# Optimization experiments

Measured on AMD Instinct MI355X. Metric: run time of the kernel, lower is better.

The kernel has to match this reference:

```python
import jax, jax.numpy as jnp
import numpy as np

N_NODES = 50000
N_EDGES = 800000
F_IN = 64
F_OUT = 64
EPS = 1e-5


def setup_inputs() -> dict:
    key = jax.random.key(0)
    ks = jax.random.split(key, 6)
    x = jax.random.normal(ks[0], (N_NODES, F_IN), dtype=jnp.float32)
    edge_index = jax.random.randint(ks[1], (2, N_EDGES), 0, N_NODES, dtype=jnp.int64)
    # pre MLP: Linear(2*F_in -> F_in); post MLP: Linear(13*F_in -> F_out); lin: Linear(F_out -> F_out)
    pre_w = jax.random.normal(ks[2], (2 * F_IN, F_IN), dtype=jnp.float32) / np.sqrt(2 * F_IN)
    pre_b = jnp.zeros((F_IN,), dtype=jnp.float32)
    post_w = jax.random.normal(ks[3], (13 * F_IN, F_OUT), dtype=jnp.float32) / np.sqrt(13 * F_IN)
    post_b = jnp.zeros((F_OUT,), dtype=jnp.float32)
    lin_w = jax.random.normal(ks[4], (F_OUT, F_OUT), dtype=jnp.float32) / np.sqrt(F_OUT)
    lin_b = jnp.zeros((F_OUT,), dtype=jnp.float32)
    return {"x": x, "edge_index": edge_index, "pre_w": pre_w, "pre_b": pre_b,
            "post_w": post_w, "post_b": post_b, "lin_w": lin_w, "lin_b": lin_b}


def _pna_conv(x, edge_index, pre_w, pre_b, post_w, post_b, lin_w, lin_b):
    n = x.shape[0]
    src = edge_index[0]  # x_j (source / neighbor)
    dst = edge_index[1]  # x_i (target / aggregation index)

    # message: pre-MLP on [x_i, x_j]  -> [E, F_in]
    h = jnp.concatenate([x[dst], x[src]], axis=-1)  # [E, 2*F_in]
    m = h @ pre_w + pre_b                            # [E, F_in]

    # degree of each target node
    deg = jax.ops.segment_sum(jnp.ones_like(src, dtype=x.dtype), dst, num_segments=n)  # [N]
    has_nb = deg > 0
    deg_c = jnp.maximum(deg, 1.0)[:, None]  # clamp(1), [N,1]

    # aggregators: mean, min, max, std (single pass over edges per reduction)
    s1 = jax.ops.segment_sum(m, dst, num_segments=n)
    s2 = jax.ops.segment_sum(m * m, dst, num_segments=n)
    mean = s1 / deg_c
    mean_sq = s2 / deg_c
    std = jnp.sqrt(jax.nn.relu(mean_sq - mean * mean) + EPS)
    mn = jax.ops.segment_min(m, dst, num_segments=n)
    mx = jax.ops.segment_max(m, dst, num_segments=n)
    mn = jnp.where(has_nb[:, None], mn, 0.0)
    mx = jnp.where(has_nb[:, None], mx, 0.0)
    aggs = jnp.concatenate([mean, mn, mx, std], axis=-1)  # [N, 4*F_in]

    # degree scalers: identity, amplification, attenuation
    # avg log-degree from the graph's degree histogram (log(deg+1), unclamped)
    avg_deg_log = jnp.mean(jnp.log(deg + 1.0))
    deg_log = jnp.log(deg_c + 1.0)  # uses clamped degree, [N,1]
    amp = deg_log / avg_deg_log
    att = avg_deg_log / deg_log
    scaled = jnp.concatenate([aggs, aggs * amp, aggs * att], axis=-1)  # [N, 12*F_in]

    # post MLP on [x, aggregated] then final linear
    out = jnp.concatenate([x, scaled], axis=-1)  # [N, 13*F_in]
    out = out @ post_w + post_b                  # [N, F_out]
    out = out @ lin_w + lin_b                    # [N, F_out]
    return out


def reference(x, edge_index, pre_w, pre_b, post_w, post_b, lin_w, lin_b):
    # eval-mode forward: dropout is identity, no loss branch
    return _pna_conv(x, edge_index, pre_w, pre_b, post_w, post_b, lin_w, lin_b)
```

## Files before the change

kernel.cpp:

```cpp
#include <hip/hip_runtime.h>
#include <math.h>
#include <stdint.h>

#define EPS 1e-5f

typedef __attribute__((ext_vector_type(8))) short bf16x8;
typedef __attribute__((ext_vector_type(4))) float f32x4;

union FragU {
    bf16x8 v;
    ushort u[8];
};

__device__ __forceinline__ ushort f2bf(float f)
{
    union { float f; uint u; } v; v.f = f;
    uint r = v.u + 0x7FFF + ((v.u >> 16) & 1);
    return (ushort)(r >> 16);
}
__device__ __forceinline__ float bf2f(ushort u)
{
    union { uint u; float f; } v; v.u = (uint)u << 16;
    return v.f;
}

#define MFMA(a, b, c) __builtin_amdgcn_mfma_f32_16x16x32_bf16((a), (b), (c), 0, 0, 0)

#define PART_BLOCKS 128

__global__ __launch_bounds__(64) void k_fuse_pack(
    const float* __restrict__ post_w, const float* __restrict__ post_b,
    const float* __restrict__ lin_w, const float* __restrict__ lin_b,
    const float* __restrict__ pre_w,
    ushort* __restrict__ Wp, float* __restrict__ bc, ushort* __restrict__ Pp)
{
    int r = blockIdx.x, j = threadIdx.x;
    if (r < 832) {
        float acc = 0.f;
        for (int k = 0; k < 64; ++k)
            acc = fmaf(post_w[r * 64 + k], lin_w[k * 64 + j], acc);
        int tile, kk;
        if (r < 64) { tile = (r >> 5) * 4 + (j >> 4); kk = r & 31; }
        else {
            int g = (r - 64) >> 8, ka = (r - 64) & 255;
            tile = 8 + (g * 8 + (ka >> 5)) * 4 + (j >> 4); kk = ka & 31;
        }
        int lane = (j & 15) | ((kk >> 3) << 4);
        Wp[tile * 512 + lane * 8 + (kk & 7)] = f2bf(acc);
    } else {
        float a = lin_b[j];
        for (int k = 0; k < 64; ++k)
            a = fmaf(post_b[k], lin_w[k * 64 + j], a);
        bc[j] = a;
        for (int idx = j; idx < 8192; idx += 64) {
            int kin = idx >> 7, o = idx & 127;
            float v = (o < 64) ? pre_w[kin * 64 + o]
                               : pre_w[(64 + kin) * 64 + (o - 64)];
            int kk = kin & 31;
            int tile = (kin >> 5) * 8 + (o >> 4);
            int lane = (o & 15) | ((kk >> 3) << 4);
            Pp[tile * 512 + lane * 8 + (kk & 7)] = f2bf(v);
        }
    }
}

__global__ __launch_bounds__(256) void k_pre(
    const float* __restrict__ x, const ushort* __restrict__ Pp,
    const float* __restrict__ pre_b,
    float* __restrict__ Af, ushort* __restrict__ Bb, int N)
{
    int w = threadIdx.x >> 6, lane = threadIdx.x & 63;
    int nb = (blockIdx.x * 4 + w) * 32;
    if (nb >= N) return;
    int lr = lane & 15, lk = lane >> 4;

    f32x4 acc[2][8] = {};
#pragma unroll
    for (int ks = 0; ks < 2; ++ks) {
        FragU A0, A1;
        {
            int r0 = min(nb + lr, N - 1);
            int r1 = min(nb + 16 + lr, N - 1);
            const float* p0 = &x[r0 * 64 + ks * 32 + lk * 8];
            const float* p1 = &x[r1 * 64 + ks * 32 + lk * 8];
            float4 a0 = *reinterpret_cast<const float4*>(p0);
            float4 a1 = *reinterpret_cast<const float4*>(p0 + 4);
            float4 c0 = *reinterpret_cast<const float4*>(p1);
            float4 c1 = *reinterpret_cast<const float4*>(p1 + 4);
            A0.u[0] = f2bf(a0.x); A0.u[1] = f2bf(a0.y);
            A0.u[2] = f2bf(a0.z); A0.u[3] = f2bf(a0.w);
            A0.u[4] = f2bf(a1.x); A0.u[5] = f2bf(a1.y);
            A0.u[6] = f2bf(a1.z); A0.u[7] = f2bf(a1.w);
            A1.u[0] = f2bf(c0.x); A1.u[1] = f2bf(c0.y);
            A1.u[2] = f2bf(c0.z); A1.u[3] = f2bf(c0.w);
            A1.u[4] = f2bf(c1.x); A1.u[5] = f2bf(c1.y);
            A1.u[6] = f2bf(c1.z); A1.u[7] = f2bf(c1.w);
        }
#pragma unroll
        for (int jt = 0; jt < 8; ++jt) {
            bf16x8 B = *reinterpret_cast<const bf16x8*>(
                &Pp[(ks * 8 + jt) * 512 + lane * 8]);
            acc[0][jt] = MFMA(A0.v, B, acc[0][jt]);
            acc[1][jt] = MFMA(A1.v, B, acc[1][jt]);
        }
    }
#pragma unroll
    for (int mt = 0; mt < 2; ++mt)
#pragma unroll
        for (int jt = 0; jt < 8; ++jt) {
            int o = jt * 16 + lr;
#pragma unroll
            for (int rg = 0; rg < 4; ++rg) {
                int r = nb + mt * 16 + lk * 4 + rg;
                if (r < N) {
                    float v = acc[mt][jt][rg];
                    if (o < 64) Af[r * 64 + o] = v + pre_b[o];
                    else        Bb[r * 64 + (o - 64)] = f2bf(v);
                }
            }
        }
}

__global__ __launch_bounds__(256) void k_hist(
    const int* __restrict__ ei, int* __restrict__ hist, int E, int N)
{
    __shared__ int lh[256];
    int t = threadIdx.x, blk = blockIdx.x;
    lh[t] = 0;
    __syncthreads();
    int chunk = (E + PART_BLOCKS - 1) / PART_BLOCKS;
    int c0 = blk * chunk, c1 = min(E, c0 + chunk);
    for (int e = c0 + t; e < c1; e += 256) {
        int dst = ei[E + e];
        if ((unsigned)dst < (unsigned)N) atomicAdd(&lh[dst >> 8], 1);
    }
    __syncthreads();
    hist[blk * 256 + t] = lh[t];
}

__global__ __launch_bounds__(128) void k_colscan(
    const int* __restrict__ hist, int* __restrict__ colscan,
    int* __restrict__ total)
{
    __shared__ int ws[2];
    int t = threadIdx.x, lane = t & 63, wv = t >> 6;
    int b = blockIdx.x;
    int v0 = hist[t * 256 + b];
    int v = v0;
#pragma unroll
    for (int off = 1; off < 64; off <<= 1) {
        int u = __shfl_up(v, off);
        if (lane >= off) v += u;
    }
    if (lane == 63) ws[wv] = v;
    __syncthreads();
    int incl = v + ((wv == 1) ? ws[0] : 0);
    colscan[t * 256 + b] = incl - v0;
    if (t == 127) total[b] = incl;
}

__global__ __launch_bounds__(256) void k_bscan(
    const int* __restrict__ total, int* __restrict__ bucketStart,
    int* __restrict__ offsets, int N)
{
    __shared__ int ws[4];
    int t = threadIdx.x, lane = t & 63, wv = t >> 6;
    int v0 = total[t];
    int v = v0;
#pragma unroll
    for (int off = 1; off < 64; off <<= 1) {
        int u = __shfl_up(v, off);
        if (lane >= off) v += u;
    }
    if (lane == 63) ws[wv] = v;
    __syncthreads();
    int add = 0;
#pragma unroll
    for (int i = 0; i < 4; ++i)
        if (i < wv) add += ws[i];
    int incl = v + add;
    bucketStart[t] = incl - v0;
    if (t == 255) {
        bucketStart[256] = incl;
        offsets[N] = incl;
    }
}

__global__ __launch_bounds__(256) void k_part(
    const int* __restrict__ ei, const int* __restrict__ colscan,
    const int* __restrict__ bucketStart, uint2* __restrict__ staged,
    int E, int N)
{
    __shared__ int cur[256];
    int t = threadIdx.x, blk = blockIdx.x;
    cur[t] = bucketStart[t] + colscan[blk * 256 + t];
    __syncthreads();
    int chunk = (E + PART_BLOCKS - 1) / PART_BLOCKS;
    int c0 = blk * chunk, c1 = min(E, c0 + chunk);
    for (int e = c0 + t; e < c1; e += 256) {
        int src = ei[e];
        int dst = ei[E + e];
        if ((unsigned)dst < (unsigned)N) {
            if ((unsigned)src >= (unsigned)N) src = 0;
            int pos = atomicAdd(&cur[dst >> 8], 1);
            staged[pos] = make_uint2((uint)src, (uint)dst);
        }
    }
}

__global__ __launch_bounds__(256) void k_place(
    const uint2* __restrict__ staged, const int* __restrict__ bucketStart,
    int* __restrict__ csr_src, int* __restrict__ offsets,
    float* __restrict__ avg_acc, int N)
{
    __shared__ int cnt[256];
    __shared__ int wsum[4];
    __shared__ float fl[4];
    int t = threadIdx.x, lane = t & 63, wv = t >> 6;
    int b = blockIdx.x;
    int s0 = bucketStart[b], s1 = bucketStart[b + 1];

    cnt[t] = 0;
    __syncthreads();
    for (int i = s0 + t; i < s1; i += 256)
        atomicAdd(&cnt[staged[i].y & 255], 1);
    __syncthreads();

    int d = cnt[t];
    int v = d;
#pragma unroll
    for (int off = 1; off < 64; off <<= 1) {
        int u = __shfl_up(v, off);
        if (lane >= off) v += u;
    }
    if (lane == 63) wsum[wv] = v;
    __syncthreads();
    int wvoff = 0;
#pragma unroll
    for (int i = 0; i < 4; ++i)
        if (i < wv) wvoff += wsum[i];
    int excl = wvoff + v - d;

    int node = b * 256 + t;
    if (node < N) offsets[node] = s0 + excl;

    float sl = (node < N) ? logf((float)d + 1.0f) : 0.f;
    for (int off = 32; off; off >>= 1) sl += __shfl_down(sl, off);
    if (lane == 0) fl[wv] = sl;

    cnt[t] = excl;
    __syncthreads();
    if (t == 0) atomicAdd(avg_acc, fl[0] + fl[1] + fl[2] + fl[3]);

    for (int i = s0 + t; i < s1; i += 256) {
        uint2 e = staged[i];
        int p = atomicAdd(&cnt[e.y & 255], 1);
        csr_src[s0 + p] = (int)e.x;
    }
}

__global__ void k_fin(const float* __restrict__ avg_acc,
                      float* __restrict__ avg_p, int N)
{
    *avg_p = *avg_acc / (float)N;
}

__global__ __launch_bounds__(256) void k_aggregate(
    const float* __restrict__ Af, const ushort* __restrict__ Bb,
    const int* __restrict__ offsets, const int* __restrict__ csr_src,
    const float* __restrict__ avg_p, ushort* __restrict__ aggs,
    float* __restrict__ amp, float* __restrict__ att, int N)
{
    int wave = threadIdx.x >> 6, lane = threadIdx.x & 63;
    int n = blockIdx.x * 4 + wave;
    if (n >= N) return;

    int off0 = offsets[n], off1 = offsets[n + 1];
    int d = off1 - off0;
    float a = Af[n * 64 + lane];

    float sum = 0.f, sq = 0.f, mn = 3.4e38f, mx = -3.4e38f;
    for (int base = off0; base < off1; base += 64) {
        int cnt = min(64, off1 - base);
        int s_idx = 0;
        if (lane < cnt) {
            s_idx = csr_src[base + lane];
            if ((unsigned)s_idx >= (unsigned)N) s_idx = 0;
        }
        int i = 0;
        for (; i + 7 < cnt; i += 8) {
            int b0 = __shfl(s_idx, i + 0), b1 = __shfl(s_idx, i + 1);
            int b2 = __shfl(s_idx, i + 2), b3 = __shfl(s_idx, i + 3);
            int b4 = __shfl(s_idx, i + 4), b5 = __shfl(s_idx, i + 5);
            int b6 = __shfl(s_idx, i + 6), b7 = __shfl(s_idx, i + 7);
            ushort u0 = Bb[b0 * 64 + lane], u1 = Bb[b1 * 64 + lane];
            ushort u2 = Bb[b2 * 64 + lane], u3 = Bb[b3 * 64 + lane];
            ushort u4 = Bb[b4 * 64 + lane], u5 = Bb[b5 * 64 + lane];
            ushort u6 = Bb[b6 * 64 + lane], u7 = Bb[b7 * 64 + lane];
            float m0 = a + bf2f(u0), m1 = a + bf2f(u1);
            float m2 = a + bf2f(u2), m3 = a + bf2f(u3);
            float m4 = a + bf2f(u4), m5 = a + bf2f(u5);
            float m6 = a + bf2f(u6), m7 = a + bf2f(u7);
            sum += m0; sq = fmaf(m0, m0, sq); mn = fminf(mn, m0); mx = fmaxf(mx, m0);
            sum += m1; sq = fmaf(m1, m1, sq); mn = fminf(mn, m1); mx = fmaxf(mx, m1);
            sum += m2; sq = fmaf(m2, m2, sq); mn = fminf(mn, m2); mx = fmaxf(mx, m2);
            sum += m3; sq = fmaf(m3, m3, sq); mn = fminf(mn, m3); mx = fmaxf(mx, m3);
            sum += m4; sq = fmaf(m4, m4, sq); mn = fminf(mn, m4); mx = fmaxf(mx, m4);
            sum += m5; sq = fmaf(m5, m5, sq); mn = fminf(mn, m5); mx = fmaxf(mx, m5);
            sum += m6; sq = fmaf(m6, m6, sq); mn = fminf(mn, m6); mx = fmaxf(mx, m6);
            sum += m7; sq = fmaf(m7, m7, sq); mn = fminf(mn, m7); mx = fmaxf(mx, m7);
        }
        for (; i < cnt; ++i) {
            int sj = __shfl(s_idx, i);
            float m = a + bf2f(Bb[sj * 64 + lane]);
            sum += m; sq = fmaf(m, m, sq); mn = fminf(mn, m); mx = fmaxf(mx, m);
        }
    }
    float dc = (d > 0) ? (float)d : 1.0f;
    float mean = sum / dc;
    float msq = sq / dc;
    float var = msq - mean * mean;
    float std = sqrtf(fmaxf(var, 0.f) + EPS);
    if (d == 0) { mn = 0.f; mx = 0.f; }

    aggs[n * 256 + lane]       = f2bf(mean);
    aggs[n * 256 + 64 + lane]  = f2bf(mn);
    aggs[n * 256 + 128 + lane] = f2bf(mx);
    aggs[n * 256 + 192 + lane] = f2bf(std);

    if (lane == 0) {
        float avg = *avg_p;
        float dlog = logf(dc + 1.0f);
        amp[n] = dlog / avg;
        att[n] = avg / dlog;
    }
}

__global__ __launch_bounds__(256) void k_out_gemm(
    const float* __restrict__ x, const ushort* __restrict__ aggs,
    const float* __restrict__ amp, const float* __restrict__ att,
    const ushort* __restrict__ Wp, const float* __restrict__ bc,
    float* __restrict__ out, int N)
{
    int w = threadIdx.x >> 6, lane = threadIdx.x & 63;
    int nb = (blockIdx.x * 4 + w) * 32;
    int lr = lane & 15, lk = lane >> 4;

    f32x4 accP[2][4] = {};
    f32x4 accA[2][4] = {};
    f32x4 accT[2][4] = {};

#pragma unroll
    for (int ks = 0; ks < 2; ++ks) {
        FragU A0, A1;
        {
            int r0 = min(nb + lr, N - 1);
            int r1 = min(nb + 16 + lr, N - 1);
            const float* p0 = &x[r0 * 64 + ks * 32 + lk * 8];
            const float* p1 = &x[r1 * 64 + ks * 32 + lk * 8];
            float4 a0 = *reinterpret_cast<const float4*>(p0);
            float4 a1 = *reinterpret_cast<const float4*>(p0 + 4);
            float4 c0 = *reinterpret_cast<const float4*>(p1);
            float4 c1 = *reinterpret_cast<const float4*>(p1 + 4);
            A0.u[0] = f2bf(a0.x); A0.u[1] = f2bf(a0.y);
            A0.u[2] = f2bf(a0.z); A0.u[3] = f2bf(a0.w);
            A0.u[4] = f2bf(a1.x); A0.u[5] = f2bf(a1.y);
            A0.u[6] = f2bf(a1.z); A0.u[7] = f2bf(a1.w);
            A1.u[0] = f2bf(c0.x); A1.u[1] = f2bf(c0.y);
            A1.u[2] = f2bf(c0.z); A1.u[3] = f2bf(c0.w);
            A1.u[4] = f2bf(c1.x); A1.u[5] = f2bf(c1.y);
            A1.u[6] = f2bf(c1.z); A1.u[7] = f2bf(c1.w);
        }
#pragma unroll
        for (int jt = 0; jt < 4; ++jt) {
            bf16x8 B = *reinterpret_cast<const bf16x8*>(
                &Wp[(ks * 4 + jt) * 512 + lane * 8]);
            accP[0][jt] = MFMA(A0.v, B, accP[0][jt]);
            accP[1][jt] = MFMA(A1.v, B, accP[1][jt]);
        }
    }

#pragma unroll 2
    for (int ks = 0; ks < 8; ++ks) {
        bf16x8 A0 = *reinterpret_cast<const bf16x8*>(
            &aggs[(size_t)(nb + lr) * 256 + ks * 32 + lk * 8]);
        bf16x8 A1 = *reinterpret_cast<const bf16x8*>(
            &aggs[(size_t)(nb + 16 + lr) * 256 + ks * 32 + lk * 8]);
        bf16x8 B0[4], B1[4], B2[4];
#pragma unroll
        for (int jt = 0; jt < 4; ++jt) {
            B0[jt] = *reinterpret_cast<const bf16x8*>(
                &Wp[(8 + (0 * 8 + ks) * 4 + jt) * 512 + lane * 8]);
            B1[jt] = *reinterpret_cast<const bf16x8*>(
                &Wp[(8 + (1 * 8 + ks) * 4 + jt) * 512 + lane * 8]);
            B2[jt] = *reinterpret_cast<const bf16x8*>(
                &Wp[(8 + (2 * 8 + ks) * 4 + jt) * 512 + lane * 8]);
        }
#pragma unroll
        for (int jt = 0; jt < 4; ++jt) {
            accP[0][jt] = MFMA(A0, B0[jt], accP[0][jt]);
            accP[1][jt] = MFMA(A1, B0[jt], accP[1][jt]);
            accA[0][jt] = MFMA(A0, B1[jt], accA[0][jt]);
            accA[1][jt] = MFMA(A1, B1[jt], accA[1][jt]);
            accT[0][jt] = MFMA(A0, B2[jt], accT[0][jt]);
            accT[1][jt] = MFMA(A1, B2[jt], accT[1][jt]);
        }
    }

#pragma unroll
    for (int mt = 0; mt < 2; ++mt) {
        int rb = nb + mt * 16 + lk * 4;
        float am[4], at[4];
#pragma unroll
        for (int rg = 0; rg < 4; ++rg) {
            am[rg] = amp[rb + rg];
            at[rg] = att[rb + rg];
        }
#pragma unroll
        for (int jt = 0; jt < 4; ++jt) {
            int j = jt * 16 + lr;
            float b = bc[j];
#pragma unroll
            for (int rg = 0; rg < 4; ++rg) {
                int r = rb + rg;
                if (r < N) {
                    out[(size_t)r * 64 + j] =
                        accP[mt][jt][rg] + am[rg] * accA[mt][jt][rg] +
                        at[rg] * accT[mt][jt][rg] + b;
                }
            }
        }
    }
}

static inline char* alignup(char* p, size_t a)
{
    return (char*)(((uintptr_t)p + a - 1) & ~(uintptr_t)(a - 1));
}

extern "C" void kernel_launch(void* const* d_in, const int* in_sizes, int n_in,
                              void* d_out, int out_size, void* d_ws, size_t ws_size,
                              hipStream_t stream)
{
    const float* x      = (const float*)d_in[0];
    const int*   ei     = (const int*)d_in[1];
    const float* pre_w  = (const float*)d_in[2];
    const float* pre_b  = (const float*)d_in[3];
    const float* post_w = (const float*)d_in[4];
    const float* post_b = (const float*)d_in[5];
    const float* lin_w  = (const float*)d_in[6];
    const float* lin_b  = (const float*)d_in[7];
    float* out = (float*)d_out;

    const int N = in_sizes[0] / 64;
    const int E = in_sizes[1] / 2;
    const int Npad = (N + 127) & ~127;
    const int NWB = Npad / 128;
    const int NBUCK = (N + 255) >> 8;
    if (N > 65536) return;

    size_t need = 0;
    auto acct = [&](size_t bytes) { need = ((need + 255) & ~(size_t)255) + bytes; };
    acct((size_t)N * 64 * 4);
    acct((size_t)N * 64 * 2);
    acct((size_t)Npad * 256 * 2);
    acct(104 * 512 * 2);
    acct(16 * 512 * 2);
    acct(64 * 4);
    acct((size_t)Npad * 4);
    acct((size_t)Npad * 4);
    acct(((size_t)N + 1) * 4);
    acct((size_t)E * 4);
    acct((size_t)E * 8);
    acct(PART_BLOCKS * 256 * 4);
    acct(PART_BLOCKS * 256 * 4);
    acct(256 * 4);
    acct(257 * 4);
    acct(4);
    acct(4);
    if (ws_size < need) return;

    char* p = (char*)d_ws;
    auto take = [&](size_t bytes) {
        p = alignup(p, 256);
        void* r = (void*)p;
        p += bytes;
        return r;
    };
    float*  Af        = (float*)take((size_t)N * 64 * 4);
    ushort* Bb        = (ushort*)take((size_t)N * 64 * 2);
    ushort* aggs      = (ushort*)take((size_t)Npad * 256 * 2);
    ushort* Wp        = (ushort*)take(104 * 512 * 2);
    ushort* Pp        = (ushort*)take(16 * 512 * 2);
    float*  bc        = (float*)take(64 * 4);
    float*  amp       = (float*)take((size_t)Npad * 4);
    float*  att       = (float*)take((size_t)Npad * 4);
    int*    offsets   = (int*)take(((size_t)N + 1) * 4);
    int*    csr_src   = (int*)take((size_t)E * 4);
    uint2*  staged    = (uint2*)take((size_t)E * 8);
    int*    hist      = (int*)take(PART_BLOCKS * 256 * 4);
    int*    colscan   = (int*)take(PART_BLOCKS * 256 * 4);
    int*    total     = (int*)take(256 * 4);
    int*    bstart    = (int*)take(257 * 4);
    float*  avg_acc   = (float*)take(4);
    float*  avg_p     = (float*)take(4);

    hipMemsetAsync(avg_acc, 0, 4, stream);

    k_fuse_pack<<<833, 64, 0, stream>>>(post_w, post_b, lin_w, lin_b, pre_w,
                                        Wp, bc, Pp);
    k_pre<<<NWB, 256, 0, stream>>>(x, Pp, pre_b, Af, Bb, N);
    k_hist<<<PART_BLOCKS, 256, 0, stream>>>(ei, hist, E, N);
    k_colscan<<<256, 128, 0, stream>>>(hist, colscan, total);
    k_bscan<<<1, 256, 0, stream>>>(total, bstart, offsets, N);
    k_part<<<PART_BLOCKS, 256, 0, stream>>>(ei, colscan, bstart, staged, E, N);
    k_place<<<NBUCK, 256, 0, stream>>>(staged, bstart, csr_src, offsets,
                                       avg_acc, N);
    k_fin<<<1, 1, 0, stream>>>(avg_acc, avg_p, N);
    k_aggregate<<<(N + 3) / 4, 256, 0, stream>>>(Af, Bb, offsets, csr_src,
                                                 avg_p, aggs, amp, att, N);
    k_out_gemm<<<NWB, 256, 0, stream>>>(x, aggs, amp, att, Wp, bc, out, N);
}
```

Baseline: 210.5 us.

## Fuse pre-GEMM with histogram, merge scans, pack staged edges, vectorize aggregation

Combines the pre-MLP GEMM and the edge histogram into one launch and packs pre_w into shared memory per block. It merges the column and bucket scans into a single-block kernel, which also zeroes the accumulator, and drops the memset and finalize kernels. Staged edges are compacted into 32-bit words holding a 16-bit src and the low dst byte. The aggregation processes two edges per wave step using 32-bit bf16 pair loads. This reduces launch count and memory traffic, but it repeats the weight packing in every block and relies on node ids fitting in 16 bits.

```diff
diff --git a/kernel.cpp b/kernel.cpp
--- a/kernel.cpp
+++ b/kernel.cpp
@@ -23,6 +23,10 @@
     union { uint u; float f; } v; v.u = (uint)u << 16;
     return v.f;
 }
+__device__ __forceinline__ uint packbf2(float lo, float hi)
+{
+    return (uint)f2bf(lo) | ((uint)f2bf(hi) << 16);
+}
 
 #define MFMA(a, b, c) __builtin_amdgcn_mfma_f32_16x16x32_bf16((a), (b), (c), 0, 0, 0)
 
@@ -31,8 +35,7 @@
 __global__ __launch_bounds__(64) void k_fuse_pack(
     const float* __restrict__ post_w, const float* __restrict__ post_b,
     const float* __restrict__ lin_w, const float* __restrict__ lin_b,
-    const float* __restrict__ pre_w,
-    ushort* __restrict__ Wp, float* __restrict__ bc, ushort* __restrict__ Pp)
+    ushort* __restrict__ Wp, float* __restrict__ bc)
 {
     int r = blockIdx.x, j = threadIdx.x;
     if (r < 832) {
@@ -52,24 +55,45 @@
         for (int k = 0; k < 64; ++k)
             a = fmaf(post_b[k], lin_w[k * 64 + j], a);
         bc[j] = a;
-        for (int idx = j; idx < 8192; idx += 64) {
-            int kin = idx >> 7, o = idx & 127;
-            float v = (o < 64) ? pre_w[kin * 64 + o]
-                               : pre_w[(64 + kin) * 64 + (o - 64)];
-            int kk = kin & 31;
-            int tile = (kin >> 5) * 8 + (o >> 4);
-            int lane = (o & 15) | ((kk >> 3) << 4);
-            Pp[tile * 512 + lane * 8 + (kk & 7)] = f2bf(v);
-        }
-    }
-}
-
-__global__ __launch_bounds__(256) void k_pre(
-    const float* __restrict__ x, const ushort* __restrict__ Pp,
-    const float* __restrict__ pre_b,
-    float* __restrict__ Af, ushort* __restrict__ Bb, int N)
-{
-    int w = threadIdx.x >> 6, lane = threadIdx.x & 63;
+    }
+}
+
+__global__ __launch_bounds__(256) void k_preh(
+    const float* __restrict__ x, const float* __restrict__ pre_w,
+    const float* __restrict__ pre_b, const int* __restrict__ ei,
+    float* __restrict__ Af, ushort* __restrict__ Bb,
+    int* __restrict__ hist, int N, int E, int NWB)
+{
+    int t = threadIdx.x;
+    if (blockIdx.x >= NWB) {
+        __shared__ int lh[256];
+        int blk = blockIdx.x - NWB;
+        lh[t] = 0;
+        __syncthreads();
+        int chunk = (E + PART_BLOCKS - 1) / PART_BLOCKS;
+        int c0 = blk * chunk, c1 = min(E, c0 + chunk);
+        for (int e = c0 + t; e < c1; e += 256) {
+            int dst = ei[E + e];
+            if ((unsigned)dst < (unsigned)N) atomicAdd(&lh[dst >> 8], 1);
+        }
+        __syncthreads();
+        hist[blk * 256 + t] = lh[t];
+        return;
+    }
+
+    __shared__ ushort pw[16 * 512];
+    for (int idx = t; idx < 8192; idx += 256) {
+        int kin = idx >> 7, o = idx & 127;
+        float v = (o < 64) ? pre_w[kin * 64 + o]
+                           : pre_w[(64 + kin) * 64 + (o - 64)];
+        int kk = kin & 31;
+        int tile = (kin >> 5) * 8 + (o >> 4);
+        int ln = (o & 15) | ((kk >> 3) << 4);
+        pw[tile * 512 + ln * 8 + (kk & 7)] = f2bf(v);
+    }
+    __syncthreads();
+
+    int w = t >> 6, lane = t & 63;
     int nb = (blockIdx.x * 4 + w) * 32;
     if (nb >= N) return;
     int lr = lane & 15, lk = lane >> 4;
@@ -99,7 +123,7 @@
 #pragma unroll
         for (int jt = 0; jt < 8; ++jt) {
             bf16x8 B = *reinterpret_cast<const bf16x8*>(
-                &Pp[(ks * 8 + jt) * 512 + lane * 8]);
+                &pw[(ks * 8 + jt) * 512 + lane * 8]);
             acc[0][jt] = MFMA(A0.v, B, acc[0][jt]);
             acc[1][jt] = MFMA(A1.v, B, acc[1][jt]);
         }
@@ -121,66 +145,43 @@
         }
 }
 
-__global__ __launch_bounds__(256) void k_hist(
-    const int* __restrict__ ei, int* __restrict__ hist, int E, int N)
-{
-    __shared__ int lh[256];
-    int t = threadIdx.x, blk = blockIdx.x;
-    lh[t] = 0;
-    __syncthreads();
-    int chunk = (E + PART_BLOCKS - 1) / PART_BLOCKS;
-    int c0 = blk * chunk, c1 = min(E, c0 + chunk);
-    for (int e = c0 + t; e < c1; e += 256) {
-        int dst = ei[E + e];
-        if ((unsigned)dst < (unsigned)N) atomicAdd(&lh[dst >> 8], 1);
-    }
-    __syncthreads();
-    hist[blk * 256 + t] = lh[t];
-}
-
-__global__ __launch_bounds__(128) void k_colscan(
+__global__ __launch_bounds__(256) void k_cscan(
     const int* __restrict__ hist, int* __restrict__ colscan,
-    int* __restrict__ total)
-{
-    __shared__ int ws[2];
-    int t = threadIdx.x, lane = t & 63, wv = t >> 6;
-    int b = blockIdx.x;
-    int v0 = hist[t * 256 + b];
-    int v = v0;
+    int* __restrict__ bucketStart, int* __restrict__ offsets,
+    float* __restrict__ avg_acc, int N)
+{
+    __shared__ int ws[4];
+    int b = threadIdx.x;
+    if (b == 0) *avg_acc = 0.f;
+
+    int run = 0;
+    for (int base = 0; base < PART_BLOCKS; base += 8) {
+        int h[8];
+#pragma unroll
+        for (int k = 0; k < 8; ++k) h[k] = hist[(base + k) * 256 + b];
+#pragma unroll
+        for (int k = 0; k < 8; ++k) {
+            colscan[(base + k) * 256 + b] = run;
+            run += h[k];
+        }
+    }
+
+    int lane = b & 63, wv = b >> 6;
+    int inc = run;
 #pragma unroll
     for (int off = 1; off < 64; off <<= 1) {
-        int u = __shfl_up(v, off);
-        if (lane >= off) v += u;
-    }
-    if (lane == 63) ws[wv] = v;
-    __syncthreads();
-    int incl = v + ((wv == 1) ? ws[0] : 0);
-    colscan[t * 256 + b] = incl - v0;
-    if (t == 127) total[b] = incl;
-}
-
-__global__ __launch_bounds__(256) void k_bscan(
-    const int* __restrict__ total, int* __restrict__ bucketStart,
-    int* __restrict__ offsets, int N)
-{
-    __shared__ int ws[4];
-    int t = threadIdx.x, lane = t & 63, wv = t >> 6;
-    int v0 = total[t];
-    int v = v0;
-#pragma unroll
-    for (int off = 1; off < 64; off <<= 1) {
-        int u = __shfl_up(v, off);
-        if (lane >= off) v += u;
-    }
-    if (lane == 63) ws[wv] = v;
+        int u = __shfl_up(inc, off);
+        if (lane >= off) inc += u;
+    }
+    if (lane == 63) ws[wv] = inc;
     __syncthreads();
     int add = 0;
 #pragma unroll
     for (int i = 0; i < 4; ++i)
         if (i < wv) add += ws[i];
-    int incl = v + add;
-    bucketStart[t] = incl - v0;
-    if (t == 255) {
+    int incl = inc + add;
+    bucketStart[b] = incl - run;
+    if (b == 255) {
         bucketStart[256] = incl;
         offsets[N] = incl;
     }
@@ -188,7 +189,7 @@
 
 __global__ __launch_bounds__(256) void k_part(
     const int* __restrict__ ei, const int* __restrict__ colscan,
-    const int* __restrict__ bucketStart, uint2* __restrict__ staged,
+    const int* __restrict__ bucketStart, uint* __restrict__ staged,
     int E, int N)
 {
     __shared__ int cur[256];
@@ -203,13 +204,13 @@
         if ((unsigned)dst < (unsigned)N) {
             if ((unsigned)src >= (unsigned)N) src = 0;
             int pos = atomicAdd(&cur[dst >> 8], 1);
-            staged[pos] = make_uint2((uint)src, (uint)dst);
+            staged[pos] = (uint)src | ((uint)(dst & 255) << 16);
         }
     }
 }
 
 __global__ __launch_bounds__(256) void k_place(
-    const uint2* __restrict__ staged, const int* __restrict__ bucketStart,
+    const uint* __restrict__ staged, const int* __restrict__ bucketStart,
     int* __restrict__ csr_src, int* __restrict__ offsets,
     float* __restrict__ avg_acc, int N)
 {
@@ -223,7 +224,7 @@
     cnt[t] = 0;
     __syncthreads();
     for (int i = s0 + t; i < s1; i += 256)
-        atomicAdd(&cnt[staged[i].y & 255], 1);
+        atomicAdd(&cnt[(staged[i] >> 16) & 255], 1);
     __syncthreads();
 
     int d = cnt[t];
@@ -253,22 +254,16 @@
     if (t == 0) atomicAdd(avg_acc, fl[0] + fl[1] + fl[2] + fl[3]);
 
     for (int i = s0 + t; i < s1; i += 256) {
-        uint2 e = staged[i];
-        int p = atomicAdd(&cnt[e.y & 255], 1);
-        csr_src[s0 + p] = (int)e.x;
-    }
-}
-
-__global__ void k_fin(const float* __restrict__ avg_acc,
-                      float* __restrict__ avg_p, int N)
-{
-    *avg_p = *avg_acc / (float)N;
+        uint ev = staged[i];
+        int p = atomicAdd(&cnt[(ev >> 16) & 255], 1);
+        csr_src[s0 + p] = (int)(ev & 0xFFFFu);
+    }
 }
 
 __global__ __launch_bounds__(256) void k_aggregate(
     const float* __restrict__ Af, const ushort* __restrict__ Bb,
     const int* __restrict__ offsets, const int* __restrict__ csr_src,
-    const float* __restrict__ avg_p, ushort* __restrict__ aggs,
+    const float* __restrict__ avg_sum, ushort* __restrict__ aggs,
     float* __restrict__ amp, float* __restrict__ att, int N)
 {
     int wave = threadIdx.x >> 6, lane = threadIdx.x & 63;
@@ -277,59 +272,70 @@
 
     int off0 = offsets[n], off1 = offsets[n + 1];
     int d = off1 - off0;
-    float a = Af[n * 64 + lane];
-
-    float sum = 0.f, sq = 0.f, mn = 3.4e38f, mx = -3.4e38f;
+    int hl = lane & 31;
+    int which = lane >> 5;
+
+    float2 a2 = *reinterpret_cast<const float2*>(&Af[(size_t)n * 64 + hl * 2]);
+
+    float s0 = 0.f, s1 = 0.f, q0 = 0.f, q1 = 0.f;
+    float mn0 = 3.4e38f, mn1 = 3.4e38f, mx0 = -3.4e38f, mx1 = -3.4e38f;
+
+#define UPD(bv)                                                         \
+    {                                                                   \
+        float m0 = a2.x + bf2f((ushort)((bv) & 0xFFFFu));               \
+        float m1 = a2.y + bf2f((ushort)((bv) >> 16));                   \
+        s0 += m0; q0 = fmaf(m0, m0, q0);                                \
+        mn0 = fminf(mn0, m0); mx0 = fmaxf(mx0, m0);                     \
+        s1 += m1; q1 = fmaf(m1, m1, q1);                                \
+        mn1 = fminf(mn1, m1); mx1 = fmaxf(mx1, m1);                     \
+    }
+
     for (int base = off0; base < off1; base += 64) {
         int cnt = min(64, off1 - base);
         int s_idx = 0;
-        if (lane < cnt) {
-            s_idx = csr_src[base + lane];
-            if ((unsigned)s_idx >= (unsigned)N) s_idx = 0;
-        }
+        if (lane < cnt) s_idx = csr_src[base + lane];
         int i = 0;
         for (; i + 7 < cnt; i += 8) {
-            int b0 = __shfl(s_idx, i + 0), b1 = __shfl(s_idx, i + 1);
-            int b2 = __shfl(s_idx, i + 2), b3 = __shfl(s_idx, i + 3);
-            int b4 = __shfl(s_idx, i + 4), b5 = __shfl(s_idx, i + 5);
-            int b6 = __shfl(s_idx, i + 6), b7 = __shfl(s_idx, i + 7);
-            ushort u0 = Bb[b0 * 64 + lane], u1 = Bb[b1 * 64 + lane];
-            ushort u2 = Bb[b2 * 64 + lane], u3 = Bb[b3 * 64 + lane];
-            ushort u4 = Bb[b4 * 64 + lane], u5 = Bb[b5 * 64 + lane];
-            ushort u6 = Bb[b6 * 64 + lane], u7 = Bb[b7 * 64 + lane];
-            float m0 = a + bf2f(u0), m1 = a + bf2f(u1);
-            float m2 = a + bf2f(u2), m3 = a + bf2f(u3);
-            float m4 = a + bf2f(u4), m5 = a + bf2f(u5);
-            float m6 = a + bf2f(u6), m7 = a + bf2f(u7);
-            sum += m0; sq = fmaf(m0, m0, sq); mn = fminf(mn, m0); mx = fmaxf(mx, m0);
-            sum += m1; sq = fmaf(m1, m1, sq); mn = fminf(mn, m1); mx = fmaxf(mx, m1);
-            sum += m2; sq = fmaf(m2, m2, sq); mn = fminf(mn, m2); mx = fmaxf(mx, m2);
-            sum += m3; sq = fmaf(m3, m3, sq); mn = fminf(mn, m3); mx = fmaxf(mx, m3);
-            sum += m4; sq = fmaf(m4, m4, sq); mn = fminf(mn, m4); mx = fmaxf(mx, m4);
-            sum += m5; sq = fmaf(m5, m5, sq); mn = fminf(mn, m5); mx = fmaxf(mx, m5);
-            sum += m6; sq = fmaf(m6, m6, sq); mn = fminf(mn, m6); mx = fmaxf(mx, m6);
-            sum += m7; sq = fmaf(m7, m7, sq); mn = fminf(mn, m7); mx = fmaxf(mx, m7);
-        }
-        for (; i < cnt; ++i) {
-            int sj = __shfl(s_idx, i);
-            float m = a + bf2f(Bb[sj * 64 + lane]);
-            sum += m; sq = fmaf(m, m, sq); mn = fminf(mn, m); mx = fmaxf(mx, m);
-        }
-    }
+            int sA = __shfl(s_idx, i + 0 + which);
+            int sB = __shfl(s_idx, i + 2 + which);
+            int sC = __shfl(s_idx, i + 4 + which);
+            int sD = __shfl(s_idx, i + 6 + which);
+            uint bA = *reinterpret_cast<const uint*>(&Bb[(size_t)sA * 64 + hl * 2]);
+            uint bB = *reinterpret_cast<const uint*>(&Bb[(size_t)sB * 64 + hl * 2]);
+            uint bC = *reinterpret_cast<const uint*>(&Bb[(size_t)sC * 64 + hl * 2]);
+            uint bD = *reinterpret_cast<const uint*>(&Bb[(size_t)sD * 64 + hl * 2]);
+            UPD(bA); UPD(bB); UPD(bC); UPD(bD);
+        }
+        for (; i < cnt; i += 2) {
+            int sj = __shfl(s_idx, i + which);
+            uint bv = *reinterpret_cast<const uint*>(&Bb[(size_t)sj * 64 + hl * 2]);
+            if ((which == 0) | (i + 1 < cnt)) UPD(bv);
+        }
+    }
+#undef UPD
+
+    s0 += __shfl_xor(s0, 32);  s1 += __shfl_xor(s1, 32);
+    q0 += __shfl_xor(q0, 32);  q1 += __shfl_xor(q1, 32);
+    mn0 = fminf(mn0, __shfl_xor(mn0, 32));
+    mn1 = fminf(mn1, __shfl_xor(mn1, 32));
+    mx0 = fmaxf(mx0, __shfl_xor(mx0, 32));
+    mx1 = fmaxf(mx1, __shfl_xor(mx1, 32));
+
     float dc = (d > 0) ? (float)d : 1.0f;
-    float mean = sum / dc;
-    float msq = sq / dc;
-    float var = msq - mean * mean;
-    float std = sqrtf(fmaxf(var, 0.f) + EPS);
-    if (d == 0) { mn = 0.f; mx = 0.f; }
-
-    aggs[n * 256 + lane]       = f2bf(mean);
-    aggs[n * 256 + 64 + lane]  = f2bf(mn);
-    aggs[n * 256 + 128 + lane] = f2bf(mx);
-    aggs[n * 256 + 192 + lane] = f2bf(std);
-
+    float mean0 = s0 / dc, mean1 = s1 / dc;
+    float std0 = sqrtf(fmaxf(q0 / dc - mean0 * mean0, 0.f) + EPS);
+    float std1 = sqrtf(fmaxf(q1 / dc - mean1 * mean1, 0.f) + EPS);
+    if (d == 0) { mn0 = 0.f; mn1 = 0.f; mx0 = 0.f; mx1 = 0.f; }
+
+    if (lane < 32) {
+        uint* ag = reinterpret_cast<uint*>(&aggs[(size_t)n * 256]);
+        ag[0 * 32 + hl] = packbf2(mean0, mean1);
+        ag[1 * 32 + hl] = packbf2(mn0, mn1);
+        ag[2 * 32 + hl] = packbf2(mx0, mx1);
+        ag[3 * 32 + hl] = packbf2(std0, std1);
+    }
     if (lane == 0) {
-        float avg = *avg_p;
+        float avg = *avg_sum / (float)N;
         float dlog = logf(dc + 1.0f);
         amp[n] = dlog / avg;
         att[n] = avg / dlog;
@@ -465,18 +471,15 @@
     acct((size_t)N * 64 * 2);
     acct((size_t)Npad * 256 * 2);
     acct(104 * 512 * 2);
-    acct(16 * 512 * 2);
     acct(64 * 4);
     acct((size_t)Npad * 4);
     acct((size_t)Npad * 4);
     acct(((size_t)N + 1) * 4);
     acct((size_t)E * 4);
-    acct((size_t)E * 8);
+    acct((size_t)E * 4);
     acct(PART_BLOCKS * 256 * 4);
     acct(PART_BLOCKS * 256 * 4);
-    acct(256 * 4);
     acct(257 * 4);
-    acct(4);
     acct(4);
     if (ws_size < need) return;
 
@@ -491,33 +494,25 @@
     ushort* Bb        = (ushort*)take((size_t)N * 64 * 2);
     ushort* aggs      = (ushort*)take((size_t)Npad * 256 * 2);
     ushort* Wp        = (ushort*)take(104 * 512 * 2);
-    ushort* Pp        = (ushort*)take(16 * 512 * 2);
     float*  bc        = (float*)take(64 * 4);
     float*  amp       = (float*)take((size_t)Npad * 4);
     float*  att       = (float*)take((size_t)Npad * 4);
     int*    offsets   = (int*)take(((size_t)N + 1) * 4);
     int*    csr_src   = (int*)take((size_t)E * 4);
-    uint2*  staged    = (uint2*)take((size_t)E * 8);
+    uint*   staged    = (uint*)take((size_t)E * 4);
     int*    hist      = (int*)take(PART_BLOCKS * 256 * 4);
     int*    colscan   = (int*)take(PART_BLOCKS * 256 * 4);
-    int*    total     = (int*)take(256 * 4);
     int*    bstart    = (int*)take(257 * 4);
     float*  avg_acc   = (float*)take(4);
-    float*  avg_p     = (float*)take(4);
-
-    hipMemsetAsync(avg_acc, 0, 4, stream);
-
-    k_fuse_pack<<<833, 64, 0, stream>>>(post_w, post_b, lin_w, lin_b, pre_w,
-                                        Wp, bc, Pp);
-    k_pre<<<NWB, 256, 0, stream>>>(x, Pp, pre_b, Af, Bb, N);
-    k_hist<<<PART_BLOCKS, 256, 0, stream>>>(ei, hist, E, N);
-    k_colscan<<<256, 128, 0, stream>>>(hist, colscan, total);
-    k_bscan<<<1, 256, 0, stream>>>(total, bstart, offsets, N);
+
+    k_preh<<<NWB + PART_BLOCKS, 256, 0, stream>>>(x, pre_w, pre_b, ei,
+                                                  Af, Bb, hist, N, E, NWB);
+    k_fuse_pack<<<833, 64, 0, stream>>>(post_w, post_b, lin_w, lin_b, Wp, bc);
+    k_cscan<<<1, 256, 0, stream>>>(hist, colscan, bstart, offsets, avg_acc, N);
     k_part<<<PART_BLOCKS, 256, 0, stream>>>(ei, colscan, bstart, staged, E, N);
     k_place<<<NBUCK, 256, 0, stream>>>(staged, bstart, csr_src, offsets,
                                        avg_acc, N);
-    k_fin<<<1, 1, 0, stream>>>(avg_acc, avg_p, N);
     k_aggregate<<<(N + 3) / 4, 256, 0, stream>>>(Af, Bb, offsets, csr_src,
-                                                 avg_p, aggs, amp, att, N);
+                                                 avg_acc, aggs, amp, att, N);
     k_out_gemm<<<NWB, 256, 0, stream>>>(x, aggs, amp, att, Wp, bc, out, N);
 }
```

After: 186.0 us. -11.6%, faster.
